# Optimization experiments

Hardware: AMD Instinct MI355X
Metric: run time of the kernel (lower is better)

## Reference

```python
import jax, jax.numpy as jnp
import numpy as np

B, S, P, D, H = 2, 4096, 1024, 1024, 16  # batch, byte seq, patches, d_model, heads


def setup_inputs() -> dict:
    key = jax.random.key(0)
    ks = jax.random.split(key, 8)
    init = 0.02
    queries = jax.random.normal(ks[0], (B, S, D), dtype=jnp.float32)
    patch_representations = jax.random.normal(ks[1], (B, P, D), dtype=jnp.float32)
    patch_boundaries = jax.random.randint(ks[2], (B, S), 0, 2, dtype=jnp.int32)
    wq = jax.random.normal(ks[3], (D, D), dtype=jnp.float32) * init
    wk = jax.random.normal(ks[4], (D, D), dtype=jnp.float32) * init
    wv = jax.random.normal(ks[5], (D, D), dtype=jnp.float32) * init
    wo = jax.random.normal(ks[6], (D, D), dtype=jnp.float32) * init
    bq = jnp.zeros((D,), jnp.float32)
    bk = jnp.zeros((D,), jnp.float32)
    bv = jnp.zeros((D,), jnp.float32)
    bo = jnp.zeros((D,), jnp.float32)
    return {"queries": queries, "patch_representations": patch_representations,
            "patch_boundaries": patch_boundaries,
            "wq": wq, "wk": wk, "wv": wv, "wo": wo,
            "bq": bq, "bk": bk, "bv": bv, "bo": bo}


def reference(queries, patch_representations, patch_boundaries,
              wq, wk, wv, wo, bq, bk, bv, bo):
    b, s, d = queries.shape
    p = patch_representations.shape[1]
    h = H
    dh = d // h
    scale = 1.0 / jnp.sqrt(jnp.asarray(dh, queries.dtype))

    # in-projections (torch Linear: x @ W.T + b)
    q = (queries @ wq.T + bq).reshape(b, s, h, dh)
    k = (patch_representations @ wk.T + bk).reshape(b, p, h, dh)
    v = (patch_representations @ wv.T + bv).reshape(b, p, h, dh)

    # scores: [b, h, s, p]
    scores = jnp.einsum('bqhd,bkhd->bhqk', q, k) * scale

    # data-dependent patch-boundary mask: byte t may attend to patch j iff j <= cumsum(boundaries)[t]
    patch_idx = jnp.cumsum(patch_boundaries, axis=1)          # [b, s]
    mask = jnp.arange(p)[None, None, :] > patch_idx[:, :, None]  # [b, s, p], True = masked
    scores = jnp.where(mask[:, None, :, :], jnp.finfo(scores.dtype).min, scores)

    attn = jax.nn.softmax(scores, axis=-1)                    # dropout inactive (eval)
    out = jnp.einsum('bhqk,bkhd->bqhd', attn, v).reshape(b, s, d)
    return out @ wo.T + bo
```

## Files before the change

### kernel.cpp

```cpp
#include <hip/hip_runtime.h>


#define B_ 2
#define S_ 4096
#define P_ 1024
#define D_ 1024
#define H_ 16
#define DH_ 64

#define NCONV 14336

typedef __attribute__((ext_vector_type(8))) short short8;
typedef __attribute__((ext_vector_type(4))) float f32x4;

#define KSCALE 0.18033688011112042f

#if __has_builtin(__builtin_amdgcn_exp2f)
#define EXP2(x) __builtin_amdgcn_exp2f(x)
#else
#define EXP2(x) exp2f(x)
#endif

static __device__ __forceinline__ unsigned short f2bf(float f) {
    unsigned int u = __float_as_uint(f);
    u += 0x7FFFu + ((u >> 16) & 1u);
    return (unsigned short)(u >> 16);
}

static __device__ __forceinline__ void gll16(const unsigned short* g,
                                             const unsigned short* l) {
    __builtin_amdgcn_global_load_lds(
        (const __attribute__((address_space(1))) unsigned int*)g,
        (__attribute__((address_space(3))) unsigned int*)l,
        16, 0, 0);
}

__global__ __launch_bounds__(256) void xattn_convert_all(
    const float* __restrict__ queries, const float* __restrict__ patches,
    const float* __restrict__ wq, const float* __restrict__ wk,
    const float* __restrict__ wv, const float* __restrict__ wo,
    unsigned short* __restrict__ qb, unsigned short* __restrict__ pb,
    unsigned short* __restrict__ wqb, unsigned short* __restrict__ wkb,
    unsigned short* __restrict__ wvb, unsigned short* __restrict__ wob,
    const int* __restrict__ bounds, int* __restrict__ pidx) {
    if (blockIdx.x >= NCONV) {
        __shared__ int sdata[256];
        int b = blockIdx.x - NCONV;
        int t = threadIdx.x;
        const int* src = bounds + b * S_ + t * 16;
        int vals[16];
        int run = 0;
#pragma unroll
        for (int i = 0; i < 16; ++i) { run += src[i]; vals[i] = run; }
        sdata[t] = run;
        __syncthreads();
        for (int off = 1; off < 256; off <<= 1) {
            int v = (t >= off) ? sdata[t - off] : 0;
            __syncthreads();
            sdata[t] += v;
            __syncthreads();
        }
        int prefix = (t > 0) ? sdata[t - 1] : 0;
        int* dst = pidx + b * S_ + t * 16;
#pragma unroll
        for (int i = 0; i < 16; ++i) dst[i] = prefix + vals[i];
        return;
    }
    const int NQ = (B_ * S_ * D_) / 4;
    const int NP = (B_ * P_ * D_) / 4;
    const int NW = (D_ * D_) / 4;
    int i = blockIdx.x * 256 + threadIdx.x;
    const float* src;
    unsigned short* dst;
    int j;
    if (i < NQ) { src = queries; dst = qb; j = i; }
    else if (i < NQ + NP) { src = patches; dst = pb; j = i - NQ; }
    else {
        int k = i - NQ - NP;
        int wsel = k >> 18;
        j = k & (NW - 1);
        if (wsel == 0) { src = wq; dst = wqb; }
        else if (wsel == 1) { src = wk; dst = wkb; }
        else if (wsel == 2) { src = wv; dst = wvb; }
        else { src = wo; dst = wob; }
    }
    float4 v = ((const float4*)src)[j];
    ushort4 o;
    o.x = f2bf(v.x); o.y = f2bf(v.y); o.z = f2bf(v.z); o.w = f2bf(v.w);
    ((ushort4*)dst)[j] = o;
}

__global__ __launch_bounds__(256) void xattn_gemm_qkv(
    const unsigned short* __restrict__ qb, const unsigned short* __restrict__ pb,
    const unsigned short* __restrict__ wqb, const unsigned short* __restrict__ wkb,
    const unsigned short* __restrict__ wvb,
    const float* __restrict__ bq, const float* __restrict__ bk,
    const float* __restrict__ bv,
    unsigned short* __restrict__ Qout, unsigned short* __restrict__ Kout,
    unsigned short* __restrict__ Vout) {
    const int K = 1024, N = 1024;
    const int byy = blockIdx.y;
    int z, my;
    if (byy < 64)      { z = 0; my = byy; }
    else if (byy < 80) { z = 1; my = byy - 64; }
    else               { z = 2; my = byy - 80; }
    const unsigned short* A = (z == 0) ? qb : pb;
    const unsigned short* W = (z == 0) ? wqb : ((z == 1) ? wkb : wvb);
    const float* bias = (z == 0) ? bq : ((z == 1) ? bk : bv);

    __shared__ unsigned short As[128 * 32];
    __shared__ unsigned short Bs[128 * 32];

    const int m0 = my * 128;
    const int n0 = blockIdx.x * 128;
    const int t = threadIdx.x;
    const int w = t >> 6;
    const int l = t & 63;
    const int fr = l & 15, fq = l >> 4;
    const int wr = w >> 1, wc = w & 1;

    const int r0s = t >> 2;
    const int cs = (t & 3) * 8;
    const unsigned short* Ap0 = A + (size_t)(m0 + r0s) * K + cs;
    const unsigned short* Ap1 = A + (size_t)(m0 + 64 + r0s) * K + cs;
    const unsigned short* Wp0 = W + (size_t)(n0 + r0s) * K + cs;
    const unsigned short* Wp1 = W + (size_t)(n0 + 64 + r0s) * K + cs;
    const unsigned short* lA0 = &As[(w * 64) * 8];
    const unsigned short* lA1 = &As[(256 + w * 64) * 8];
    const unsigned short* lB0 = &Bs[(w * 64) * 8];
    const unsigned short* lB1 = &Bs[(256 + w * 64) * 8];

    f32x4 acc[4][4];
#pragma unroll
    for (int i = 0; i < 4; ++i)
#pragma unroll
        for (int j = 0; j < 4; ++j) acc[i][j] = (f32x4){0.f, 0.f, 0.f, 0.f};

    for (int k0 = 0; k0 < K; k0 += 32) {
        gll16(Ap0 + k0, lA0);
        gll16(Ap1 + k0, lA1);
        gll16(Wp0 + k0, lB0);
        gll16(Wp1 + k0, lB1);
        __syncthreads();
        short8 af[4], bf[4];
#pragma unroll
        for (int i = 0; i < 4; ++i)
            af[i] = *(const short8*)&As[(wr * 64 + i * 16 + fr) * 32 + fq * 8];
#pragma unroll
        for (int j = 0; j < 4; ++j)
            bf[j] = *(const short8*)&Bs[(wc * 64 + j * 16 + fr) * 32 + fq * 8];
#pragma unroll
        for (int i = 0; i < 4; ++i)
#pragma unroll
            for (int j = 0; j < 4; ++j)
                acc[i][j] = __builtin_amdgcn_mfma_f32_16x16x32_bf16(af[i], bf[j], acc[i][j], 0, 0, 0);
        __syncthreads();
    }

#pragma unroll
    for (int j = 0; j < 4; ++j) {
        int n = n0 + wc * 64 + j * 16 + fr;
        float bvv = bias[n];
#pragma unroll
        for (int i = 0; i < 4; ++i) {
            int mbase = m0 + wr * 64 + i * 16 + fq * 4;
#pragma unroll
            for (int r = 0; r < 4; ++r) {
                float val = acc[i][j][r] + bvv;
                int m = mbase + r;
                if (z == 0) {
                    Qout[(size_t)m * N + n] = f2bf(val * KSCALE);
                } else if (z == 1) {
                    Kout[(size_t)m * N + n] = f2bf(val);
                } else {
                    int bb = m >> 10, c = m & (P_ - 1);
                    int hh = n >> 6, d = n & 63;
                    int cl = c & 63;
                    int cp = (c & 960) | (((cl & 15) << 2) | (cl >> 4));
                    Vout[(((size_t)(bb * H_ + hh)) * 64 + d) * P_ + cp] = f2bf(val);
                }
            }
        }
    }
}

__global__ __launch_bounds__(256) void xattn_gemm_o(
    const unsigned short* __restrict__ A,
    const unsigned short* __restrict__ W,
    const float* __restrict__ bias,
    float* __restrict__ Cout) {
    const int K = 1024, N = 1024;
    __shared__ unsigned short As[128 * 32];
    __shared__ unsigned short Bs[128 * 32];

    const int m0 = blockIdx.y * 128;
    const int n0 = blockIdx.x * 128;
    const int t = threadIdx.x;
    const int w = t >> 6;
    const int l = t & 63;
    const int fr = l & 15, fq = l >> 4;
    const int wr = w >> 1, wc = w & 1;

    const int r0s = t >> 2;
    const int cs = (t & 3) * 8;
    const unsigned short* Ap0 = A + (size_t)(m0 + r0s) * K + cs;
    const unsigned short* Ap1 = A + (size_t)(m0 + 64 + r0s) * K + cs;
    const unsigned short* Wp0 = W + (size_t)(n0 + r0s) * K + cs;
    const unsigned short* Wp1 = W + (size_t)(n0 + 64 + r0s) * K + cs;
    const unsigned short* lA0 = &As[(w * 64) * 8];
    const unsigned short* lA1 = &As[(256 + w * 64) * 8];
    const unsigned short* lB0 = &Bs[(w * 64) * 8];
    const unsigned short* lB1 = &Bs[(256 + w * 64) * 8];

    f32x4 acc[4][4];
#pragma unroll
    for (int i = 0; i < 4; ++i)
#pragma unroll
        for (int j = 0; j < 4; ++j) acc[i][j] = (f32x4){0.f, 0.f, 0.f, 0.f};

    for (int k0 = 0; k0 < K; k0 += 32) {
        gll16(Ap0 + k0, lA0);
        gll16(Ap1 + k0, lA1);
        gll16(Wp0 + k0, lB0);
        gll16(Wp1 + k0, lB1);
        __syncthreads();
        short8 af[4], bf[4];
#pragma unroll
        for (int i = 0; i < 4; ++i)
            af[i] = *(const short8*)&As[(wr * 64 + i * 16 + fr) * 32 + fq * 8];
#pragma unroll
        for (int j = 0; j < 4; ++j)
            bf[j] = *(const short8*)&Bs[(wc * 64 + j * 16 + fr) * 32 + fq * 8];
#pragma unroll
        for (int i = 0; i < 4; ++i)
#pragma unroll
            for (int j = 0; j < 4; ++j)
                acc[i][j] = __builtin_amdgcn_mfma_f32_16x16x32_bf16(af[i], bf[j], acc[i][j], 0, 0, 0);
        __syncthreads();
    }

#pragma unroll
    for (int j = 0; j < 4; ++j) {
        int n = n0 + wc * 64 + j * 16 + fr;
        float bvv = bias[n];
#pragma unroll
        for (int i = 0; i < 4; ++i) {
            int mbase = m0 + wr * 64 + i * 16 + fq * 4;
#pragma unroll
            for (int r = 0; r < 4; ++r)
                Cout[(size_t)(mbase + r) * N + n] = acc[i][j][r] + bvv;
        }
    }
}

__global__ __launch_bounds__(256) void xattn_attn_mfma(
    const unsigned short* __restrict__ Qb,
    const unsigned short* __restrict__ Kb,
    const unsigned short* __restrict__ Vtb,
    const int* __restrict__ pidx,
    unsigned short* __restrict__ Ob) {
    __shared__ unsigned short Ks[2][64 * 64];
    __shared__ unsigned short Vs[2][64 * 64];
    __shared__ unsigned short Ps[64 * 64];

    const int q0 = (63 - blockIdx.x) * 64;
    const int h = blockIdx.y;
    const int b = blockIdx.z;
    const int t = threadIdx.x;
    const int w = t >> 6, l = t & 63;
    const int fr = l & 15, fq = l >> 4;

    const unsigned short* qrow =
        Qb + (size_t)(b * S_ + q0 + w * 16 + fr) * D_ + h * DH_ + fq * 8;
    short8 qf0 = *(const short8*)qrow;
    short8 qf1 = *(const short8*)(qrow + 32);

    int prow[4];
#pragma unroll
    for (int r = 0; r < 4; ++r)
        prow[r] = pidx[b * S_ + q0 + w * 16 + fq * 4 + r];
    const int limit = pidx[b * S_ + q0 + 63];
    const int ntiles = (min(limit, P_ - 1) + 64) >> 6;
    const int nfull = (pidx[b * S_ + q0] + 1) >> 6;

    float lsum[4] = {0.f, 0.f, 0.f, 0.f};
    f32x4 oacc[4];
#pragma unroll
    for (int nt = 0; nt < 4; ++nt) oacc[nt] = (f32x4){0.f, 0.f, 0.f, 0.f};

    const int srow = l >> 3;
    const int g = (l & 7) ^ srow;
    const unsigned short* kbase = Kb + (size_t)(b * P_) * D_ + h * DH_;
    const unsigned short* vbase = Vtb + (size_t)(b * H_ + h) * 64 * P_;
    const unsigned short* kp0 = kbase + (size_t)(w * 16 + srow) * D_ + g * 8;
    const unsigned short* kp1 = kp0 + (size_t)8 * D_;
    const unsigned short* vp0 = vbase + (size_t)(w * 16 + srow) * P_ + g * 8;
    const unsigned short* vp1 = vp0 + (size_t)8 * P_;

    gll16(kp0, &Ks[0][w * 1024]);
    gll16(kp1, &Ks[0][w * 1024 + 512]);
    gll16(vp0, &Vs[0][w * 1024]);
    gll16(vp1, &Vs[0][w * 1024 + 512]);
    kp0 += (size_t)64 * D_; kp1 += (size_t)64 * D_;
    vp0 += 64; vp1 += 64;

    const int sw = (fq ^ (fr & 7)) * 8;
    int cur = 0;

    for (int kt = 0; kt < ntiles; ++kt) {
        __builtin_amdgcn_s_barrier();
        if (kt + 1 < ntiles) {
            const int nb = cur ^ 1;
            gll16(kp0, &Ks[nb][w * 1024]);
            gll16(kp1, &Ks[nb][w * 1024 + 512]);
            gll16(vp0, &Vs[nb][w * 1024]);
            gll16(vp1, &Vs[nb][w * 1024 + 512]);
            kp0 += (size_t)64 * D_; kp1 += (size_t)64 * D_;
            vp0 += 64; vp1 += 64;
            asm volatile("s_waitcnt vmcnt(4)" ::: "memory");
        } else {
            asm volatile("s_waitcnt vmcnt(0)" ::: "memory");
        }
        __builtin_amdgcn_sched_barrier(0);
        __builtin_amdgcn_s_barrier();

        const unsigned short* Kc = Ks[cur];
        const unsigned short* Vc = Vs[cur];
        const int c0 = kt * 64;
        const int maskme = (kt >= nfull);

        f32x4 s[4];
        __builtin_amdgcn_s_setprio(1);
#pragma unroll
        for (int nt = 0; nt < 4; ++nt) {
            short8 kf0 = *(const short8*)&Kc[(nt * 16 + fr) * 64 + sw];
            short8 kf1 = *(const short8*)&Kc[(nt * 16 + fr) * 64 + (sw ^ 32)];
            f32x4 a = (f32x4){0.f, 0.f, 0.f, 0.f};
            a = __builtin_amdgcn_mfma_f32_16x16x32_bf16(qf0, kf0, a, 0, 0, 0);
            a = __builtin_amdgcn_mfma_f32_16x16x32_bf16(qf1, kf1, a, 0, 0, 0);
            s[nt] = a;
        }
        __builtin_amdgcn_s_setprio(0);

        if (maskme) {
#pragma unroll
            for (int nt = 0; nt < 4; ++nt) {
                const int col = c0 + nt * 16 + fr;
#pragma unroll
                for (int r = 0; r < 4; ++r) {
                    float p = EXP2(s[nt][r]);
                    p = (col > prow[r]) ? 0.f : p;
                    s[nt][r] = p;
                    lsum[r] += p;
                }
            }
        } else {
#pragma unroll
            for (int nt = 0; nt < 4; ++nt) {
#pragma unroll
                for (int r = 0; r < 4; ++r) {
                    float p = EXP2(s[nt][r]);
                    s[nt][r] = p;
                    lsum[r] += p;
                }
            }
        }

#pragma unroll
        for (int r = 0; r < 4; ++r) {
            uint2 pk;
            pk.x = __builtin_amdgcn_perm(__float_as_uint(s[1][r]),
                                         __float_as_uint(s[0][r]), 0x07060302u);
            pk.y = __builtin_amdgcn_perm(__float_as_uint(s[3][r]),
                                         __float_as_uint(s[2][r]), 0x07060302u);
            const int pr = w * 16 + fq * 4 + r;
            const int pg = (((fr >> 1) ^ (pr & 7)) << 3) | ((fr & 1) << 2);
            *(uint2*)&Ps[pr * 64 + pg] = pk;
        }

        const int prr = (w * 16 + fr) * 64;
        short8 pf0 = *(const short8*)&Ps[prr + sw];
        short8 pf1 = *(const short8*)&Ps[prr + (sw ^ 32)];
        __builtin_amdgcn_s_setprio(1);
#pragma unroll
        for (int nt = 0; nt < 4; ++nt) {
            short8 vf0 = *(const short8*)&Vc[(nt * 16 + fr) * 64 + sw];
            short8 vf1 = *(const short8*)&Vc[(nt * 16 + fr) * 64 + (sw ^ 32)];
            oacc[nt] = __builtin_amdgcn_mfma_f32_16x16x32_bf16(pf0, vf0, oacc[nt], 0, 0, 0);
            oacc[nt] = __builtin_amdgcn_mfma_f32_16x16x32_bf16(pf1, vf1, oacc[nt], 0, 0, 0);
        }
        __builtin_amdgcn_s_setprio(0);

        cur ^= 1;
    }

#pragma unroll
    for (int off = 1; off < 16; off <<= 1) {
#pragma unroll
        for (int r = 0; r < 4; ++r)
            lsum[r] += __shfl_xor(lsum[r], off);
    }
    float inv[4];
#pragma unroll
    for (int r = 0; r < 4; ++r) inv[r] = 1.0f / lsum[r];

    unsigned short* obase = Ob + (size_t)(b * S_ + q0 + w * 16) * D_ + h * DH_;
#pragma unroll
    for (int nt = 0; nt < 4; ++nt)
#pragma unroll
        for (int r = 0; r < 4; ++r)
            obase[(size_t)(fq * 4 + r) * D_ + nt * 16 + fr] =
                f2bf(oacc[nt][r] * inv[r]);
}

extern "C" void kernel_launch(void* const* d_in, const int* in_sizes, int n_in,
                              void* d_out, int out_size, void* d_ws, size_t ws_size,
                              hipStream_t stream) {
    const float* queries = (const float*)d_in[0];
    const float* patches = (const float*)d_in[1];
    const int* bounds    = (const int*)d_in[2];
    const float* wq = (const float*)d_in[3];
    const float* wk = (const float*)d_in[4];
    const float* wv = (const float*)d_in[5];
    const float* wo = (const float*)d_in[6];
    const float* bq = (const float*)d_in[7];
    const float* bk = (const float*)d_in[8];
    const float* bv = (const float*)d_in[9];
    const float* bo = (const float*)d_in[10];
    float* out = (float*)d_out;

    char* ws = (char*)d_ws;
    unsigned short* qb    = (unsigned short*)(ws + 0);
    unsigned short* pb    = (unsigned short*)(ws + 16777216);
    unsigned short* wqb   = (unsigned short*)(ws + 20971520);
    unsigned short* wkb   = (unsigned short*)(ws + 23068672);
    unsigned short* wvb   = (unsigned short*)(ws + 25165824);
    unsigned short* wob   = (unsigned short*)(ws + 27262976);
    unsigned short* Qbf   = (unsigned short*)(ws + 29360128);
    unsigned short* Kbf   = (unsigned short*)(ws + 46137344);
    unsigned short* Vtb   = (unsigned short*)(ws + 50331648);
    unsigned short* attnb = (unsigned short*)(ws + 54525952);
    int* pidx             = (int*)(ws + 71303168);

    xattn_convert_all<<<dim3(NCONV + B_), 256, 0, stream>>>(
        queries, patches, wq, wk, wv, wo, qb, pb, wqb, wkb, wvb, wob,
        bounds, pidx);
    xattn_gemm_qkv<<<dim3(8, 96), 256, 0, stream>>>(
        qb, pb, wqb, wkb, wvb, bq, bk, bv, Qbf, Kbf, Vtb);
    xattn_attn_mfma<<<dim3(S_ / 64, H_, B_), 256, 0, stream>>>(
        Qbf, Kbf, Vtb, pidx, attnb);
    xattn_gemm_o<<<dim3(8, 64), 256, 0, stream>>>(attnb, wob, bo, out);
}
```

Baseline: 236.1 us.

## Double-buffer LDS in projection GEMMs with XOR swizzle and prefetch

Both projection GEMM kernels now use two LDS buffers. The next K-tile's global-to-LDS loads are issued before the current tile is computed, with explicit vmcnt waits and raw barriers replacing the syncthreads pair. The LDS column index is XOR-swizzled to reduce bank conflicts on fragment reads, and wave priority is raised around the MFMA block. This aims to hide global load latency behind compute, at the cost of doubled LDS use and fragile hand-written waitcnt logic.

```diff
diff --git a/kernel.cpp b/kernel.cpp
--- a/kernel.cpp
+++ b/kernel.cpp
@@ -108,8 +108,8 @@
     const unsigned short* W = (z == 0) ? wqb : ((z == 1) ? wkb : wvb);
     const float* bias = (z == 0) ? bq : ((z == 1) ? bk : bv);
 
-    __shared__ unsigned short As[128 * 32];
-    __shared__ unsigned short Bs[128 * 32];
+    __shared__ unsigned short As[2][128 * 32];
+    __shared__ unsigned short Bs[2][128 * 32];
 
     const int m0 = my * 128;
     const int n0 = blockIdx.x * 128;
@@ -120,15 +120,13 @@
     const int wr = w >> 1, wc = w & 1;
 
     const int r0s = t >> 2;
-    const int cs = (t & 3) * 8;
-    const unsigned short* Ap0 = A + (size_t)(m0 + r0s) * K + cs;
-    const unsigned short* Ap1 = A + (size_t)(m0 + 64 + r0s) * K + cs;
-    const unsigned short* Wp0 = W + (size_t)(n0 + r0s) * K + cs;
-    const unsigned short* Wp1 = W + (size_t)(n0 + 64 + r0s) * K + cs;
-    const unsigned short* lA0 = &As[(w * 64) * 8];
-    const unsigned short* lA1 = &As[(256 + w * 64) * 8];
-    const unsigned short* lB0 = &Bs[(w * 64) * 8];
-    const unsigned short* lB1 = &Bs[(256 + w * 64) * 8];
+    const int csw = ((t & 3) ^ ((t >> 3) & 3)) * 8;
+    const unsigned short* Ap0 = A + (size_t)(m0 + r0s) * K + csw;
+    const unsigned short* Ap1 = A + (size_t)(m0 + 64 + r0s) * K + csw;
+    const unsigned short* Wp0 = W + (size_t)(n0 + r0s) * K + csw;
+    const unsigned short* Wp1 = W + (size_t)(n0 + 64 + r0s) * K + csw;
+
+    const int gsw = (fq ^ ((fr >> 1) & 3)) * 8;
 
     f32x4 acc[4][4];
 #pragma unroll
@@ -136,25 +134,43 @@
 #pragma unroll
         for (int j = 0; j < 4; ++j) acc[i][j] = (f32x4){0.f, 0.f, 0.f, 0.f};
 
-    for (int k0 = 0; k0 < K; k0 += 32) {
-        gll16(Ap0 + k0, lA0);
-        gll16(Ap1 + k0, lA1);
-        gll16(Wp0 + k0, lB0);
-        gll16(Wp1 + k0, lB1);
-        __syncthreads();
+    gll16(Ap0, &As[0][w * 512]);
+    gll16(Ap1, &As[0][2048 + w * 512]);
+    gll16(Wp0, &Bs[0][w * 512]);
+    gll16(Wp1, &Bs[0][2048 + w * 512]);
+
+    for (int kt = 0; kt < 32; ++kt) {
+        __builtin_amdgcn_s_barrier();
+        if (kt + 1 < 32) {
+            const int nb = (kt + 1) & 1;
+            const int ks = (kt + 1) * 32;
+            gll16(Ap0 + ks, &As[nb][w * 512]);
+            gll16(Ap1 + ks, &As[nb][2048 + w * 512]);
+            gll16(Wp0 + ks, &Bs[nb][w * 512]);
+            gll16(Wp1 + ks, &Bs[nb][2048 + w * 512]);
+            asm volatile("s_waitcnt vmcnt(4)" ::: "memory");
+        } else {
+            asm volatile("s_waitcnt vmcnt(0)" ::: "memory");
+        }
+        __builtin_amdgcn_sched_barrier(0);
+        __builtin_amdgcn_s_barrier();
+
+        const unsigned short* Ac = As[kt & 1];
+        const unsigned short* Bc = Bs[kt & 1];
         short8 af[4], bf[4];
 #pragma unroll
         for (int i = 0; i < 4; ++i)
-            af[i] = *(const short8*)&As[(wr * 64 + i * 16 + fr) * 32 + fq * 8];
+            af[i] = *(const short8*)&Ac[(wr * 64 + i * 16 + fr) * 32 + gsw];
 #pragma unroll
         for (int j = 0; j < 4; ++j)
-            bf[j] = *(const short8*)&Bs[(wc * 64 + j * 16 + fr) * 32 + fq * 8];
+            bf[j] = *(const short8*)&Bc[(wc * 64 + j * 16 + fr) * 32 + gsw];
+        __builtin_amdgcn_s_setprio(1);
 #pragma unroll
         for (int i = 0; i < 4; ++i)
 #pragma unroll
             for (int j = 0; j < 4; ++j)
                 acc[i][j] = __builtin_amdgcn_mfma_f32_16x16x32_bf16(af[i], bf[j], acc[i][j], 0, 0, 0);
-        __syncthreads();
+        __builtin_amdgcn_s_setprio(0);
     }
 
 #pragma unroll
@@ -190,8 +206,8 @@
     const float* __restrict__ bias,
     float* __restrict__ Cout) {
     const int K = 1024, N = 1024;
-    __shared__ unsigned short As[128 * 32];
-    __shared__ unsigned short Bs[128 * 32];
+    __shared__ unsigned short As[2][128 * 32];
+    __shared__ unsigned short Bs[2][128 * 32];
 
     const int m0 = blockIdx.y * 128;
     const int n0 = blockIdx.x * 128;
@@ -202,15 +218,13 @@
     const int wr = w >> 1, wc = w & 1;
 
     const int r0s = t >> 2;
-    const int cs = (t & 3) * 8;
-    const unsigned short* Ap0 = A + (size_t)(m0 + r0s) * K + cs;
-    const unsigned short* Ap1 = A + (size_t)(m0 + 64 + r0s) * K + cs;
-    const unsigned short* Wp0 = W + (size_t)(n0 + r0s) * K + cs;
-    const unsigned short* Wp1 = W + (size_t)(n0 + 64 + r0s) * K + cs;
-    const unsigned short* lA0 = &As[(w * 64) * 8];
-    const unsigned short* lA1 = &As[(256 + w * 64) * 8];
-    const unsigned short* lB0 = &Bs[(w * 64) * 8];
-    const unsigned short* lB1 = &Bs[(256 + w * 64) * 8];
+    const int csw = ((t & 3) ^ ((t >> 3) & 3)) * 8;
+    const unsigned short* Ap0 = A + (size_t)(m0 + r0s) * K + csw;
+    const unsigned short* Ap1 = A + (size_t)(m0 + 64 + r0s) * K + csw;
+    const unsigned short* Wp0 = W + (size_t)(n0 + r0s) * K + csw;
+    const unsigned short* Wp1 = W + (size_t)(n0 + 64 + r0s) * K + csw;
+
+    const int gsw = (fq ^ ((fr >> 1) & 3)) * 8;
 
     f32x4 acc[4][4];
 #pragma unroll
@@ -218,25 +232,43 @@
 #pragma unroll
         for (int j = 0; j < 4; ++j) acc[i][j] = (f32x4){0.f, 0.f, 0.f, 0.f};
 
-    for (int k0 = 0; k0 < K; k0 += 32) {
-        gll16(Ap0 + k0, lA0);
-        gll16(Ap1 + k0, lA1);
-        gll16(Wp0 + k0, lB0);
-        gll16(Wp1 + k0, lB1);
-        __syncthreads();
+    gll16(Ap0, &As[0][w * 512]);
+    gll16(Ap1, &As[0][2048 + w * 512]);
+    gll16(Wp0, &Bs[0][w * 512]);
+    gll16(Wp1, &Bs[0][2048 + w * 512]);
+
+    for (int kt = 0; kt < 32; ++kt) {
+        __builtin_amdgcn_s_barrier();
+        if (kt + 1 < 32) {
+            const int nb = (kt + 1) & 1;
+            const int ks = (kt + 1) * 32;
+            gll16(Ap0 + ks, &As[nb][w * 512]);
+            gll16(Ap1 + ks, &As[nb][2048 + w * 512]);
+            gll16(Wp0 + ks, &Bs[nb][w * 512]);
+            gll16(Wp1 + ks, &Bs[nb][2048 + w * 512]);
+            asm volatile("s_waitcnt vmcnt(4)" ::: "memory");
+        } else {
+            asm volatile("s_waitcnt vmcnt(0)" ::: "memory");
+        }
+        __builtin_amdgcn_sched_barrier(0);
+        __builtin_amdgcn_s_barrier();
+
+        const unsigned short* Ac = As[kt & 1];
+        const unsigned short* Bc = Bs[kt & 1];
         short8 af[4], bf[4];
 #pragma unroll
         for (int i = 0; i < 4; ++i)
-            af[i] = *(const short8*)&As[(wr * 64 + i * 16 + fr) * 32 + fq * 8];
+            af[i] = *(const short8*)&Ac[(wr * 64 + i * 16 + fr) * 32 + gsw];
 #pragma unroll
         for (int j = 0; j < 4; ++j)
-            bf[j] = *(const short8*)&Bs[(wc * 64 + j * 16 + fr) * 32 + fq * 8];
+            bf[j] = *(const short8*)&Bc[(wc * 64 + j * 16 + fr) * 32 + gsw];
+        __builtin_amdgcn_s_setprio(1);
 #pragma unroll
         for (int i = 0; i < 4; ++i)
 #pragma unroll
             for (int j = 0; j < 4; ++j)
                 acc[i][j] = __builtin_amdgcn_mfma_f32_16x16x32_bf16(af[i], bf[j], acc[i][j], 0, 0, 0);
-        __syncthreads();
+        __builtin_amdgcn_s_setprio(0);
     }
 
 #pragma unroll
```

Result: no change. 235.7 us (-0.2%).
